# Performance work log

Hardware: AMD Instinct MI355X
Metric: run time of the kernel (lower is better)

## Reference

```python
import jax, jax.numpy as jnp
import numpy as np

B, S, E, H, D = 64, 512, 512, 8, 64  # batch, n_steps, embedding_size, head_count, QKV_dim

def setup_inputs() -> dict:
    key = jax.random.key(0)
    ks = jax.random.split(key, 7)
    x = jax.random.normal(ks[0], (B, S, E), dtype=jnp.float32)
    mask = jax.random.randint(ks[1], (B, S), 0, 2).astype(jnp.float32)  # 1 = masked out
    WQ = jax.random.normal(ks[2], (H, E, D), dtype=jnp.float32) * 0.1
    WK = jax.random.normal(ks[3], (H, E, D), dtype=jnp.float32) * 0.1
    WV = jax.random.normal(ks[4], (H, E, D), dtype=jnp.float32) * 0.1
    BE = jax.random.normal(ks[5], (S, E), dtype=jnp.float32) * 0.1
    WO = jax.random.normal(ks[6], (H * D, E), dtype=jnp.float32) * 0.1
    return {"x": x, "mask": mask, "WQ": WQ, "WK": WK, "WV": WV, "BE": BE, "WO": WO}

def reference(x, mask, WQ, WK, WV, BE, WO):
    # add learned positional bias
    h = x + BE  # [B,S,E]
    # per-head projections, vectorized over heads
    Q = jnp.einsum('bse,hed->bhsd', h, WQ)
    K = jnp.einsum('bse,hed->bhsd', h, WK)
    V = jnp.einsum('bse,hed->bhsd', h, WV)
    # NOTE: original scales by sqrt(embedding_size), not sqrt(QKV_dim)
    scores = jnp.einsum('bhsd,bhtd->bhst', Q, K) / np.sqrt(E).astype(np.float32)
    # additive mask trick: mask tiled over query dim, key positions masked where mask==1
    scores = scores - mask[:, None, None, :] * 1e10
    alpha = jax.nn.softmax(scores, axis=-1)  # [B,H,S,S]
    attn = jnp.einsum('bhst,bhtd->bhsd', alpha, V)  # [B,H,S,D]
    # concat heads along feature dim -> [B,S,H*D], then output projection
    attn = jnp.transpose(attn, (0, 2, 1, 3)).reshape(x.shape[0], x.shape[1], -1)
    return attn @ WO  # [B,S,E]
```

## Files before the change

kernel.cpp:

```cpp
#include <hip/hip_runtime.h>
#include <hip/hip_bf16.h>


#define Bn 64
#define Sn 512
#define En 512
#define Hn 8
#define Dn 64

typedef __attribute__((ext_vector_type(8))) short s8v;
typedef __attribute__((ext_vector_type(4))) float f4v;

__device__ __forceinline__ unsigned short f2bf(float f) {
    union { float f; unsigned int u; } v; v.f = f;
    unsigned int u = v.u;
    u += 0x7fffu + ((u >> 16) & 1u);
    return (unsigned short)(u >> 16);
}

__device__ __forceinline__ void async16(const unsigned short* g, unsigned short* l) {
    __builtin_amdgcn_global_load_lds((const __attribute__((address_space(1))) void*)g,
                                     (__attribute__((address_space(3))) void*)l, 16, 0, 0);
}
__device__ __forceinline__ void async4(const float* g, float* l) {
    __builtin_amdgcn_global_load_lds((const __attribute__((address_space(1))) void*)g,
                                     (__attribute__((address_space(3))) void*)l, 4, 0, 0);
}

__global__ __launch_bounds__(256) void prep_h(const float* __restrict__ x,
                                              const float* __restrict__ BE,
                                              unsigned short* __restrict__ hbf) {
    int i = (blockIdx.x * 256 + threadIdx.x) * 4;
    int se = i % (Sn * En);
    float4 a = *(const float4*)(x + i);
    float4 b = *(const float4*)(BE + se);
    ushort4 o;
    o.x = f2bf(a.x + b.x); o.y = f2bf(a.y + b.y);
    o.z = f2bf(a.z + b.z); o.w = f2bf(a.w + b.w);
    *(ushort4*)(hbf + i) = o;
}

__global__ __launch_bounds__(256) void prep_w(const float* __restrict__ WQ,
                                              const float* __restrict__ WK,
                                              const float* __restrict__ WV,
                                              const float* __restrict__ WO,
                                              unsigned short* __restrict__ Wqkvt,
                                              unsigned short* __restrict__ WOt) {
    int idx = blockIdx.x * 256 + threadIdx.x;
    const int NW = 3 * Hn * Dn * En;
    if (idx < NW) {
        int e = idx & 511;
        int d = (idx >> 9) & 63;
        int h = (idx >> 15) & 7;
        int m = idx >> 18;
        const float* W = (m == 0) ? WQ : (m == 1) ? WK : WV;
        Wqkvt[idx] = f2bf(W[(h * En + e) * Dn + d]);
    } else {
        int j = idx - NW;
        int n = j & 511;
        int e = j >> 9;
        WOt[j] = f2bf(WO[n * En + e]);
    }
}

__global__ __launch_bounds__(256) void qkv_gemm(const unsigned short* __restrict__ hbf,
                                                const unsigned short* __restrict__ Wqkvt,
                                                unsigned short* __restrict__ Qo,
                                                unsigned short* __restrict__ Ko,
                                                unsigned short* __restrict__ Vt) {
    int nb = blockIdx.x, mb = blockIdx.y;
    __shared__ __align__(16) unsigned short At[2][128 * 64];
    __shared__ __align__(16) unsigned short Bt[2][128 * 64];
    int tid = threadIdx.x;
    int w = tid >> 6, lane = tid & 63, quad = lane >> 4, l16 = lane & 15;
    int wr = w >> 1, wc = w & 1;
    int lrow = lane >> 3;
    int lseg = ((lane & 7) ^ lrow) * 8;
    bool swapQK = (nb < 8);

    f4v acc[4][4];
#pragma unroll
    for (int i = 0; i < 4; i++)
#pragma unroll
        for (int n = 0; n < 4; n++) acc[i][n] = (f4v){0.f, 0.f, 0.f, 0.f};

    const unsigned short* Ag = hbf + (size_t)mb * 128 * 512;
    const unsigned short* Bg = Wqkvt + (size_t)nb * 128 * 512;

#pragma unroll
    for (int i = 0; i < 4; i++) {
        int r0 = w * 32 + i * 8;
        async16(Ag + (r0 + lrow) * 512 + lseg, &At[0][r0 * 64]);
        async16(Bg + (r0 + lrow) * 512 + lseg, &Bt[0][r0 * 64]);
    }

    int cur = 0;
    for (int kc = 0; kc < 8; kc++) {
        if (kc < 7) {
            int nxt = cur ^ 1;
#pragma unroll
            for (int i = 0; i < 4; i++) {
                int r0 = w * 32 + i * 8;
                async16(Ag + (r0 + lrow) * 512 + (kc + 1) * 64 + lseg, &At[nxt][r0 * 64]);
                async16(Bg + (r0 + lrow) * 512 + (kc + 1) * 64 + lseg, &Bt[nxt][r0 * 64]);
            }
            asm volatile("s_waitcnt vmcnt(8)" ::: "memory");
        } else {
            asm volatile("s_waitcnt vmcnt(0)" ::: "memory");
        }
        __builtin_amdgcn_s_barrier();

#pragma unroll
        for (int ks = 0; ks < 2; ks++) {
            int sw = ((ks * 4 + quad) ^ (l16 & 7)) * 8;
            s8v a[4], b[4];
#pragma unroll
            for (int i = 0; i < 4; i++)
                a[i] = *(const s8v*)&At[cur][(wr * 64 + i * 16 + l16) * 64 + sw];
#pragma unroll
            for (int n = 0; n < 4; n++)
                b[n] = *(const s8v*)&Bt[cur][(wc * 64 + n * 16 + l16) * 64 + sw];
            if (swapQK) {
#pragma unroll
                for (int i = 0; i < 4; i++)
#pragma unroll
                    for (int n = 0; n < 4; n++)
                        acc[i][n] = __builtin_amdgcn_mfma_f32_16x16x32_bf16(b[n], a[i], acc[i][n], 0, 0, 0);
            } else {
#pragma unroll
                for (int i = 0; i < 4; i++)
#pragma unroll
                    for (int n = 0; n < 4; n++)
                        acc[i][n] = __builtin_amdgcn_mfma_f32_16x16x32_bf16(a[i], b[n], acc[i][n], 0, 0, 0);
            }
        }
        asm volatile("s_waitcnt lgkmcnt(0)" ::: "memory");
        __builtin_amdgcn_s_barrier();
        cur ^= 1;
    }

    int mat = nb >> 2;
    int h = (nb & 3) * 2 + wc;
    int b = mb >> 2;
    int s0 = (mb & 3) * 128 + wr * 64;
    const float qscale = 0.06375873f;

    if (mat < 2) {
        unsigned short* op = (mat == 0) ? Qo : Ko;
        float sc = (mat == 0) ? qscale : 1.0f;
#pragma unroll
        for (int i = 0; i < 4; i++)
#pragma unroll
            for (int n = 0; n < 4; n++) {
                int s = s0 + i * 16 + l16;
                int d0 = n * 16 + quad * 4;
                ushort4 pk;
                pk.x = f2bf(acc[i][n][0] * sc);
                pk.y = f2bf(acc[i][n][1] * sc);
                pk.z = f2bf(acc[i][n][2] * sc);
                pk.w = f2bf(acc[i][n][3] * sc);
                *(ushort4*)&op[(size_t)((b * Hn + h) * Sn + s) * Dn + d0] = pk;
            }
    } else {
#pragma unroll
        for (int i = 0; i < 4; i++)
#pragma unroll
            for (int n = 0; n < 4; n++) {
                int d = n * 16 + l16;
                int s = s0 + i * 16 + quad * 4;
                ushort4 pk;
                pk.x = f2bf(acc[i][n][0]); pk.y = f2bf(acc[i][n][1]);
                pk.z = f2bf(acc[i][n][2]); pk.w = f2bf(acc[i][n][3]);
                *(ushort4*)&Vt[(size_t)((b * Hn + h) * Dn + d) * Sn + s] = pk;
            }
    }
}

__global__ __launch_bounds__(256) void attn_kernel(const unsigned short* __restrict__ Q,
                                                   const unsigned short* __restrict__ K,
                                                   const unsigned short* __restrict__ Vt,
                                                   const float* __restrict__ mask,
                                                   unsigned short* __restrict__ attn) {
    int qhalf = blockIdx.x, bh = blockIdx.y;
    int h = bh & 7, b = bh >> 3;
    __shared__ __align__(16) unsigned short Kc[64 * 64];
    __shared__ __align__(16) unsigned short Vc[64 * 64];
    __shared__ __align__(16) unsigned short Ps[4][4 * 16 * 64];
    __shared__ float maskv[64];
    int tid = threadIdx.x;
    int w = tid >> 6, lane = tid & 63, quad = lane >> 4, l16 = lane & 15;
    int l7 = l16 & 7;

    const unsigned short* Qg = Q + (size_t)(bh * Sn + qhalf * 256) * Dn;
    const unsigned short* Kg = K + (size_t)(bh * Sn) * Dn;
    const unsigned short* Vg = Vt + (size_t)(bh * Dn) * Sn;

    s8v aq[4][2];
#pragma unroll
    for (int i = 0; i < 4; i++)
#pragma unroll
        for (int ks = 0; ks < 2; ks++)
            aq[i][ks] = *(const s8v*)&Qg[((w * 4 + i) * 16 + l16) * 64 + ks * 32 + quad * 8];

    f4v acc[4][4];
    float psum[4] = {0.f, 0.f, 0.f, 0.f};
#pragma unroll
    for (int i = 0; i < 4; i++)
#pragma unroll
        for (int n = 0; n < 4; n++) acc[i][n] = (f4v){0.f, 0.f, 0.f, 0.f};

    int srow0 = w * 16 + (lane >> 3);
    int srow1 = srow0 + 8;
    int gseg0 = ((lane & 7) ^ (srow0 & 7)) * 8;
    int gseg1 = ((lane & 7) ^ (srow1 & 7)) * 8;
    unsigned short* kdst0 = &Kc[(w * 16) * 64];
    unsigned short* kdst1 = &Kc[(w * 16 + 8) * 64];
    unsigned short* vdst0 = &Vc[(w * 16) * 64];
    unsigned short* vdst1 = &Vc[(w * 16 + 8) * 64];

    unsigned short* Pw = Ps[w];
    int wbase = l16 * 64 + (quad & 1) * 4;
    const float cM = -1.4426950409e10f;

    for (int kc = 0; kc < 8; kc++) {
        __syncthreads();
        async16(Kg + (kc * 64 + srow0) * 64 + gseg0, kdst0);
        async16(Kg + (kc * 64 + srow1) * 64 + gseg1, kdst1);
        async16(Vg + srow0 * 512 + kc * 64 + gseg0, vdst0);
        async16(Vg + srow1 * 512 + kc * 64 + gseg1, vdst1);
        if (w == 0) async4(mask + b * Sn + kc * 64 + lane, maskv);
        __syncthreads();

#pragma unroll
        for (int n = 0; n < 4; n++) {
            s8v bk0 = *(const s8v*)&Kc[(n * 16 + l16) * 64 + (quad ^ l7) * 8];
            s8v bk1 = *(const s8v*)&Kc[(n * 16 + l16) * 64 + ((4 + quad) ^ l7) * 8];
            float4 mv = *(const float4*)&maskv[n * 16 + quad * 4];
            float m0 = mv.x * cM, m1 = mv.y * cM, m2 = mv.z * cM, m3 = mv.w * cM;
            int wseg = ((n * 2 + (quad >> 1)) ^ l7) * 8;
            f4v sacc[4];
#pragma unroll
            for (int i = 0; i < 4; i++) {
                sacc[i] = __builtin_amdgcn_mfma_f32_16x16x32_bf16(
                              bk0, aq[i][0], (f4v){0.f, 0.f, 0.f, 0.f}, 0, 0, 0);
                sacc[i] = __builtin_amdgcn_mfma_f32_16x16x32_bf16(
                              bk1, aq[i][1], sacc[i], 0, 0, 0);
            }
#pragma unroll
            for (int i = 0; i < 4; i++) {
                unsigned int u0 = __float_as_uint(__builtin_amdgcn_exp2f(sacc[i][0] + m0));
                unsigned int u1 = __float_as_uint(__builtin_amdgcn_exp2f(sacc[i][1] + m1));
                unsigned int u2 = __float_as_uint(__builtin_amdgcn_exp2f(sacc[i][2] + m2));
                unsigned int u3 = __float_as_uint(__builtin_amdgcn_exp2f(sacc[i][3] + m3));
                psum[i] += __uint_as_float(u0 & 0xffff0000u) + __uint_as_float(u1 & 0xffff0000u)
                         + __uint_as_float(u2 & 0xffff0000u) + __uint_as_float(u3 & 0xffff0000u);
                uint2 pk;
                pk.x = (u0 >> 16) | (u1 & 0xffff0000u);
                pk.y = (u2 >> 16) | (u3 & 0xffff0000u);
                *(uint2*)&Pw[(i << 10) + wbase + wseg] = pk;
            }
        }

#pragma unroll
        for (int ks = 0; ks < 2; ks++) {
            int sw = ((ks * 4 + quad) ^ l7) * 8;
            s8v ap[4];
#pragma unroll
            for (int i = 0; i < 4; i++)
                ap[i] = *(const s8v*)&Pw[(i << 10) + l16 * 64 + sw];
#pragma unroll
            for (int n = 0; n < 4; n++) {
                s8v bv = *(const s8v*)&Vc[(n * 16 + l16) * 64 + sw];
#pragma unroll
                for (int i = 0; i < 4; i++)
                    acc[i][n] = __builtin_amdgcn_mfma_f32_16x16x32_bf16(ap[i], bv, acc[i][n], 0, 0, 0);
            }
        }
    }

#pragma unroll
    for (int i = 0; i < 4; i++) {
        float s = psum[i];
        s += __shfl_xor(s, 16, 64);
        s += __shfl_xor(s, 32, 64);
        float inv[4];
#pragma unroll
        for (int r = 0; r < 4; r++)
            inv[r] = 1.0f / __shfl(s, quad * 4 + r, 64);
#pragma unroll
        for (int n = 0; n < 4; n++)
#pragma unroll
            for (int r = 0; r < 4; r++) {
                int query = qhalf * 256 + (w * 4 + i) * 16 + quad * 4 + r;
                int col = h * 64 + n * 16 + l16;
                attn[(size_t)(b * Sn + query) * (Hn * Dn) + col] = f2bf(acc[i][n][r] * inv[r]);
            }
    }
}

__global__ __launch_bounds__(256) void outproj(const unsigned short* __restrict__ attn,
                                               const unsigned short* __restrict__ WOt,
                                               float* __restrict__ out) {
    int nb = blockIdx.x, mb = blockIdx.y;
    __shared__ __align__(16) unsigned short At[2][128 * 64];
    __shared__ __align__(16) unsigned short Bt[2][128 * 64];
    int tid = threadIdx.x;
    int w = tid >> 6, lane = tid & 63, quad = lane >> 4, l16 = lane & 15;
    int wr = w >> 1, wc = w & 1;
    int lrow = lane >> 3;
    int lseg = ((lane & 7) ^ lrow) * 8;

    f4v acc[4][4];
#pragma unroll
    for (int i = 0; i < 4; i++)
#pragma unroll
        for (int n = 0; n < 4; n++) acc[i][n] = (f4v){0.f, 0.f, 0.f, 0.f};

    const unsigned short* Ag = attn + (size_t)mb * 128 * 512;
    const unsigned short* Bg = WOt + (size_t)nb * 128 * 512;

#pragma unroll
    for (int i = 0; i < 4; i++) {
        int r0 = w * 32 + i * 8;
        async16(Ag + (r0 + lrow) * 512 + lseg, &At[0][r0 * 64]);
        async16(Bg + (r0 + lrow) * 512 + lseg, &Bt[0][r0 * 64]);
    }

    int cur = 0;
    for (int kc = 0; kc < 8; kc++) {
        if (kc < 7) {
            int nxt = cur ^ 1;
#pragma unroll
            for (int i = 0; i < 4; i++) {
                int r0 = w * 32 + i * 8;
                async16(Ag + (r0 + lrow) * 512 + (kc + 1) * 64 + lseg, &At[nxt][r0 * 64]);
                async16(Bg + (r0 + lrow) * 512 + (kc + 1) * 64 + lseg, &Bt[nxt][r0 * 64]);
            }
            asm volatile("s_waitcnt vmcnt(8)" ::: "memory");
        } else {
            asm volatile("s_waitcnt vmcnt(0)" ::: "memory");
        }
        __builtin_amdgcn_s_barrier();

#pragma unroll
        for (int ks = 0; ks < 2; ks++) {
            int sw = ((ks * 4 + quad) ^ (l16 & 7)) * 8;
            s8v a[4], b[4];
#pragma unroll
            for (int i = 0; i < 4; i++)
                a[i] = *(const s8v*)&At[cur][(wr * 64 + i * 16 + l16) * 64 + sw];
#pragma unroll
            for (int n = 0; n < 4; n++)
                b[n] = *(const s8v*)&Bt[cur][(wc * 64 + n * 16 + l16) * 64 + sw];
#pragma unroll
            for (int i = 0; i < 4; i++)
#pragma unroll
                for (int n = 0; n < 4; n++)
                    acc[i][n] = __builtin_amdgcn_mfma_f32_16x16x32_bf16(b[n], a[i], acc[i][n], 0, 0, 0);
        }
        asm volatile("s_waitcnt lgkmcnt(0)" ::: "memory");
        __builtin_amdgcn_s_barrier();
        cur ^= 1;
    }
#pragma unroll
    for (int i = 0; i < 4; i++)
#pragma unroll
        for (int n = 0; n < 4; n++) {
            int row = mb * 128 + wr * 64 + i * 16 + l16;
            int col = nb * 128 + wc * 64 + n * 16 + quad * 4;
            float4 o;
            o.x = acc[i][n][0]; o.y = acc[i][n][1];
            o.z = acc[i][n][2]; o.w = acc[i][n][3];
            *(float4*)&out[(size_t)row * 512 + col] = o;
        }
}

extern "C" void kernel_launch(void* const* d_in, const int* in_sizes, int n_in,
                              void* d_out, int out_size, void* d_ws, size_t ws_size,
                              hipStream_t stream) {
    const float* x    = (const float*)d_in[0];
    const float* mask = (const float*)d_in[1];
    const float* WQ   = (const float*)d_in[2];
    const float* WK   = (const float*)d_in[3];
    const float* WV   = (const float*)d_in[4];
    const float* BE   = (const float*)d_in[5];
    const float* WO   = (const float*)d_in[6];
    float* out = (float*)d_out;

    char* ws = (char*)d_ws;
    unsigned short* hbf   = (unsigned short*)(ws);
    unsigned short* Wqkvt = (unsigned short*)(ws + 33554432);
    unsigned short* WOt   = (unsigned short*)(ws + 35127296);
    unsigned short* Qp    = (unsigned short*)(ws + 35651584);
    unsigned short* Kp    = (unsigned short*)(ws + 69206016);
    unsigned short* Vtp   = (unsigned short*)(ws + 102760448);
    unsigned short* attnp = (unsigned short*)(ws + 136314880);

    prep_h<<<16384, 256, 0, stream>>>(x, BE, hbf);
    prep_w<<<4096, 256, 0, stream>>>(WQ, WK, WV, WO, Wqkvt, WOt);
    qkv_gemm<<<dim3(12, 256), 256, 0, stream>>>(hbf, Wqkvt, Qp, Kp, Vtp);
    attn_kernel<<<dim3(2, 512), 256, 0, stream>>>(Qp, Kp, Vtp, mask, attnp);
    outproj<<<dim3(4, 256), 256, 0, stream>>>(attnp, WOt, out);
}
```

Measured before the change: 304.4 us.

## Restructure QKV GEMM into 256x256 tiles with phased prefetch and block swizzle

Rewrites the QKV projection GEMM to use 512-thread blocks computing 256x256 output tiles instead of 128x128. Each K step is split into four phases that interleave async global-to-LDS loads with MFMA work, with tuned vmcnt gates and s_setprio around the MFMA bursts. A block-index swizzle groups blocks to improve L2 reuse of the A and B tiles. This raises per-block data reuse and overlaps memory with compute, at the cost of more registers, 128KB of LDS and fewer, larger blocks.

Result: faster. 292.0 us (-4.1%).

```diff
diff --git a/kernel.cpp b/kernel.cpp
--- a/kernel.cpp
+++ b/kernel.cpp
@@ -63,115 +63,157 @@
     }
 }
 
-__global__ __launch_bounds__(256) void qkv_gemm(const unsigned short* __restrict__ hbf,
-                                                const unsigned short* __restrict__ Wqkvt,
-                                                unsigned short* __restrict__ Qo,
-                                                unsigned short* __restrict__ Ko,
-                                                unsigned short* __restrict__ Vt) {
-    int nb = blockIdx.x, mb = blockIdx.y;
-    __shared__ __align__(16) unsigned short At[2][128 * 64];
-    __shared__ __align__(16) unsigned short Bt[2][128 * 64];
+__device__ __forceinline__ void mfma8(const s8v& a0k0, const s8v& a0k1,
+                                      const s8v& a1k0, const s8v& a1k1,
+                                      f4v* acc0, f4v* acc1,
+                                      const s8v (&bq)[4][2], bool sw) {
+    if (sw) {
+#pragma unroll
+        for (int n = 0; n < 4; n++) {
+            acc0[n] = __builtin_amdgcn_mfma_f32_16x16x32_bf16(bq[n][0], a0k0, acc0[n], 0, 0, 0);
+            acc0[n] = __builtin_amdgcn_mfma_f32_16x16x32_bf16(bq[n][1], a0k1, acc0[n], 0, 0, 0);
+            acc1[n] = __builtin_amdgcn_mfma_f32_16x16x32_bf16(bq[n][0], a1k0, acc1[n], 0, 0, 0);
+            acc1[n] = __builtin_amdgcn_mfma_f32_16x16x32_bf16(bq[n][1], a1k1, acc1[n], 0, 0, 0);
+        }
+    } else {
+#pragma unroll
+        for (int n = 0; n < 4; n++) {
+            acc0[n] = __builtin_amdgcn_mfma_f32_16x16x32_bf16(a0k0, bq[n][0], acc0[n], 0, 0, 0);
+            acc0[n] = __builtin_amdgcn_mfma_f32_16x16x32_bf16(a0k1, bq[n][1], acc0[n], 0, 0, 0);
+            acc1[n] = __builtin_amdgcn_mfma_f32_16x16x32_bf16(a1k0, bq[n][0], acc1[n], 0, 0, 0);
+            acc1[n] = __builtin_amdgcn_mfma_f32_16x16x32_bf16(a1k1, bq[n][1], acc1[n], 0, 0, 0);
+        }
+    }
+}
+
+__global__ __launch_bounds__(512, 2) void qkv_gemm(const unsigned short* __restrict__ hbf,
+                                                   const unsigned short* __restrict__ Wqkvt,
+                                                   unsigned short* __restrict__ Qo,
+                                                   unsigned short* __restrict__ Ko,
+                                                   unsigned short* __restrict__ Vt) {
+    __shared__ __align__(16) unsigned short As[2][16384];
+    __shared__ __align__(16) unsigned short Bs[2][16384];
+
+    int lin = blockIdx.y * 6 + blockIdx.x;
+    int swz = (lin & 7) * 96 + (lin >> 3);
+    int mb = swz / 6, nbv = swz - mb * 6;
+
     int tid = threadIdx.x;
-    int w = tid >> 6, lane = tid & 63, quad = lane >> 4, l16 = lane & 15;
-    int wr = w >> 1, wc = w & 1;
-    int lrow = lane >> 3;
-    int lseg = ((lane & 7) ^ lrow) * 8;
-    bool swapQK = (nb < 8);
-
-    f4v acc[4][4];
-#pragma unroll
-    for (int i = 0; i < 4; i++)
+    int w = tid >> 6, lane = tid & 63, quad = lane >> 4, l16 = lane & 15, l7 = l16 & 7;
+    int wr = w >> 2, wcn = w & 3;
+
+    const unsigned short* Ag = hbf + (size_t)mb * 256 * 512;
+    const unsigned short* Bg = Wqkvt + (size_t)nbv * 256 * 512;
+
+    int colbase = nbv * 256 + wcn * 64;
+    bool swapQK = colbase < 1024;
+
+    int ha = (lane >> 3) & 1;
+    int ca = w * 4 + (lane >> 4);
+    int aG0 = (ca + 128 * ha) * 512 + ((lane & 7) ^ (ca & 7)) * 8;
+    int rb0 = w * 8 + (lane >> 3);
+    int bG0 = rb0 * 512 + ((lane & 7) ^ (rb0 & 7)) * 8;
+
+    int arow = 2 * l16 + wr;
+    int aseg0 = (quad ^ l7) * 8;
+    int aseg1 = ((4 + quad) ^ l7) * 8;
+
+    f4v acc[8][4];
+#pragma unroll
+    for (int i = 0; i < 8; i++)
 #pragma unroll
         for (int n = 0; n < 4; n++) acc[i][n] = (f4v){0.f, 0.f, 0.f, 0.f};
-
-    const unsigned short* Ag = hbf + (size_t)mb * 128 * 512;
-    const unsigned short* Bg = Wqkvt + (size_t)nb * 128 * 512;
-
-#pragma unroll
-    for (int i = 0; i < 4; i++) {
-        int r0 = w * 32 + i * 8;
-        async16(Ag + (r0 + lrow) * 512 + lseg, &At[0][r0 * 64]);
-        async16(Bg + (r0 + lrow) * 512 + lseg, &Bt[0][r0 * 64]);
-    }
-
-    int cur = 0;
-    for (int kc = 0; kc < 8; kc++) {
-        if (kc < 7) {
-            int nxt = cur ^ 1;
-#pragma unroll
-            for (int i = 0; i < 4; i++) {
-                int r0 = w * 32 + i * 8;
-                async16(Ag + (r0 + lrow) * 512 + (kc + 1) * 64 + lseg, &At[nxt][r0 * 64]);
-                async16(Bg + (r0 + lrow) * 512 + (kc + 1) * 64 + lseg, &Bt[nxt][r0 * 64]);
-            }
-            asm volatile("s_waitcnt vmcnt(8)" ::: "memory");
-        } else {
-            asm volatile("s_waitcnt vmcnt(0)" ::: "memory");
-        }
-        __builtin_amdgcn_s_barrier();
-
-#pragma unroll
-        for (int ks = 0; ks < 2; ks++) {
-            int sw = ((ks * 4 + quad) ^ (l16 & 7)) * 8;
-            s8v a[4], b[4];
-#pragma unroll
-            for (int i = 0; i < 4; i++)
-                a[i] = *(const s8v*)&At[cur][(wr * 64 + i * 16 + l16) * 64 + sw];
-#pragma unroll
-            for (int n = 0; n < 4; n++)
-                b[n] = *(const s8v*)&Bt[cur][(wc * 64 + n * 16 + l16) * 64 + sw];
-            if (swapQK) {
-#pragma unroll
-                for (int i = 0; i < 4; i++)
-#pragma unroll
-                    for (int n = 0; n < 4; n++)
-                        acc[i][n] = __builtin_amdgcn_mfma_f32_16x16x32_bf16(b[n], a[i], acc[i][n], 0, 0, 0);
-            } else {
-#pragma unroll
-                for (int i = 0; i < 4; i++)
-#pragma unroll
-                    for (int n = 0; n < 4; n++)
-                        acc[i][n] = __builtin_amdgcn_mfma_f32_16x16x32_bf16(a[i], b[n], acc[i][n], 0, 0, 0);
-            }
-        }
-        asm volatile("s_waitcnt lgkmcnt(0)" ::: "memory");
-        __builtin_amdgcn_s_barrier();
-        cur ^= 1;
-    }
-
-    int mat = nb >> 2;
-    int h = (nb & 3) * 2 + wc;
-    int b = mb >> 2;
-    int s0 = (mb & 3) * 128 + wr * 64;
+    s8v bq[4][2];
+
+#define STA8(o_, p_, kt_) async16(Ag + aG0 + (p_) * 16384 + (kt_) * 64, &As[o_][(p_) * 4096 + w * 512])
+#define STB8(o_, q_, kt_) async16(Bg + bG0 + (q_) * 32768 + (kt_) * 64, &Bs[o_][(q_) * 4096 + w * 512])
+
+#define PHASE8(P, STAGES, GATE)                                                   \
+    do {                                                                          \
+        if ((P) == 0) {                                                           \
+            _Pragma("unroll")                                                     \
+            for (int n = 0; n < 4; n++) {                                         \
+                int br = (wcn * 64 + n * 16 + l16) * 64;                          \
+                bq[n][0] = *(const s8v*)&Bs_s[br + aseg0];                        \
+                bq[n][1] = *(const s8v*)&Bs_s[br + aseg1];                        \
+            }                                                                     \
+        }                                                                         \
+        s8v a0k0 = *(const s8v*)&As_s[(((P) * 2 + 0) * 32 + arow) * 64 + aseg0];  \
+        s8v a0k1 = *(const s8v*)&As_s[(((P) * 2 + 0) * 32 + arow) * 64 + aseg1];  \
+        s8v a1k0 = *(const s8v*)&As_s[(((P) * 2 + 1) * 32 + arow) * 64 + aseg0];  \
+        s8v a1k1 = *(const s8v*)&As_s[(((P) * 2 + 1) * 32 + arow) * 64 + aseg1];  \
+        STAGES;                                                                   \
+        __builtin_amdgcn_s_barrier();                                             \
+        asm volatile("s_waitcnt lgkmcnt(0)" ::: "memory");                        \
+        __builtin_amdgcn_s_setprio(1);                                            \
+        mfma8(a0k0, a0k1, a1k0, a1k1, &acc[(P) * 2][0], &acc[(P) * 2 + 1][0], bq, swapQK); \
+        __builtin_amdgcn_s_setprio(0);                                            \
+        GATE;                                                                     \
+        __builtin_amdgcn_s_barrier();                                             \
+    } while (0)
+
+    STB8(0, 0, 0); STB8(0, 1, 0); STB8(0, 2, 0); STB8(0, 3, 0);
+    STA8(0, 0, 0); STA8(0, 1, 0); STA8(0, 2, 0); STA8(0, 3, 0);
+    asm volatile("s_waitcnt vmcnt(0)" ::: "memory");
+    __builtin_amdgcn_s_barrier();
+
+    for (int k = 0; k < 7; k++) {
+        int s = k & 1, o = s ^ 1, kt = k + 1;
+        const unsigned short* As_s = &As[s][0];
+        const unsigned short* Bs_s = &Bs[s][0];
+        PHASE8(0, { STB8(o, 0, kt); STB8(o, 1, kt); STA8(o, 0, kt); },
+               asm volatile("s_waitcnt vmcnt(6)" ::: "memory"));
+        PHASE8(1, { STB8(o, 2, kt); STA8(o, 1, kt); },
+               asm volatile("s_waitcnt vmcnt(6)" ::: "memory"));
+        PHASE8(2, { STB8(o, 3, kt); STA8(o, 2, kt); },
+               asm volatile("s_waitcnt vmcnt(7)" ::: "memory"));
+        PHASE8(3, { STA8(o, 3, kt); },
+               asm volatile("s_waitcnt vmcnt(2)" ::: "memory"));
+    }
+    {
+        const unsigned short* As_s = &As[1][0];
+        const unsigned short* Bs_s = &Bs[1][0];
+        PHASE8(0, {}, asm volatile("s_waitcnt vmcnt(3)" ::: "memory"));
+        PHASE8(1, {}, asm volatile("s_waitcnt vmcnt(1)" ::: "memory"));
+        PHASE8(2, {}, asm volatile("s_waitcnt vmcnt(0)" ::: "memory"));
+        PHASE8(3, {}, (void)0);
+    }
+#undef PHASE8
+#undef STA8
+#undef STB8
+
+    int mat = colbase >> 9;
+    int h = (colbase >> 6) & 7;
+    int b_idx = mb >> 1;
     const float qscale = 0.06375873f;
 
-    if (mat < 2) {
+    if (swapQK) {
         unsigned short* op = (mat == 0) ? Qo : Ko;
         float sc = (mat == 0) ? qscale : 1.0f;
 #pragma unroll
-        for (int i = 0; i < 4; i++)
+        for (int mi = 0; mi < 8; mi++)
 #pragma unroll
             for (int n = 0; n < 4; n++) {
-                int s = s0 + i * 16 + l16;
+                int s_ = (mb & 1) * 256 + wr * 128 + mi * 16 + l16;
                 int d0 = n * 16 + quad * 4;
                 ushort4 pk;
-                pk.x = f2bf(acc[i][n][0] * sc);
-                pk.y = f2bf(acc[i][n][1] * sc);
-                pk.z = f2bf(acc[i][n][2] * sc);
-                pk.w = f2bf(acc[i][n][3] * sc);
-                *(ushort4*)&op[(size_t)((b * Hn + h) * Sn + s) * Dn + d0] = pk;
+                pk.x = f2bf(acc[mi][n][0] * sc);
+                pk.y = f2bf(acc[mi][n][1] * sc);
+                pk.z = f2bf(acc[mi][n][2] * sc);
+                pk.w = f2bf(acc[mi][n][3] * sc);
+                *(ushort4*)&op[(size_t)((b_idx * Hn + h) * Sn + s_) * Dn + d0] = pk;
             }
     } else {
 #pragma unroll
-        for (int i = 0; i < 4; i++)
+        for (int mi = 0; mi < 8; mi++)
 #pragma unroll
             for (int n = 0; n < 4; n++) {
                 int d = n * 16 + l16;
-                int s = s0 + i * 16 + quad * 4;
+                int srow = (mb & 1) * 256 + wr * 128 + mi * 16 + quad * 4;
                 ushort4 pk;
-                pk.x = f2bf(acc[i][n][0]); pk.y = f2bf(acc[i][n][1]);
-                pk.z = f2bf(acc[i][n][2]); pk.w = f2bf(acc[i][n][3]);
-                *(ushort4*)&Vt[(size_t)((b * Hn + h) * Dn + d) * Sn + s] = pk;
+                pk.x = f2bf(acc[mi][n][0]); pk.y = f2bf(acc[mi][n][1]);
+                pk.z = f2bf(acc[mi][n][2]); pk.w = f2bf(acc[mi][n][3]);
+                *(ushort4*)&Vt[(size_t)((b_idx * Hn + h) * Dn + d) * Sn + srow] = pk;
             }
     }
 }
@@ -398,7 +440,7 @@
 
     prep_h<<<16384, 256, 0, stream>>>(x, BE, hbf);
     prep_w<<<4096, 256, 0, stream>>>(WQ, WK, WV, WO, Wqkvt, WOt);
-    qkv_gemm<<<dim3(12, 256), 256, 0, stream>>>(hbf, Wqkvt, Qp, Kp, Vtp);
+    qkv_gemm<<<dim3(6, 128), 512, 0, stream>>>(hbf, Wqkvt, Qp, Kp, Vtp);
     attn_kernel<<<dim3(2, 512), 256, 0, stream>>>(Qp, Kp, Vtp, mask, attnp);
     outproj<<<dim3(4, 256), 256, 0, stream>>>(attnp, WOt, out);
 }
```
